# Kernel tuning notes

Hardware: AMD Instinct MI355X
Metric: run time of the kernel (lower is better)

The kernel has to match this reference:

```python
import jax, jax.numpy as jnp
import numpy as np

B, N, NPOINT, NSAMPLE = 16, 4096, 1024, 32
IN_CH = 3
MLP = [64, 64, 128]
EPS = 1e-5


def setup_inputs() -> dict:
    key = jax.random.key(0)
    ks = jax.random.split(key, 16)
    inp = {
        "xyz": jax.random.normal(ks[0], (B, N, 3), jnp.float32),
        "points": jax.random.normal(ks[1], (B, N, IN_CH), jnp.float32),
        "fps_idx": jax.random.randint(ks[2], (B, NPOINT), 0, N, jnp.int64),
    }
    last = IN_CH + 3
    for li, out_ch in enumerate(MLP):
        kw, kb, kg, kt = jax.random.split(jax.random.fold_in(key, 100 + li), 4)
        inp[f"w{li}"] = jax.random.normal(kw, (out_ch, last), jnp.float32) * (1.0 / np.sqrt(last))
        inp[f"b{li}"] = jax.random.normal(kb, (out_ch,), jnp.float32) * 0.01
        inp[f"g{li}"] = 1.0 + 0.1 * jax.random.normal(kg, (out_ch,), jnp.float32)
        inp[f"t{li}"] = 0.1 * jax.random.normal(kt, (out_ch,), jnp.float32)
        last = out_ch
    return inp


def _gather(x, idx):
    # x: [B, N, C], idx: [B, ...] -> [B, ..., C]
    return jax.vmap(lambda xb, ib: xb[ib])(x, idx)


def _conv_bn_relu(x, w, b, g, t):
    # x: [B, S, K, Cin]; 1x1 conv == channel matmul; BN in training mode (batch stats)
    y = jnp.einsum('bskc,oc->bsko', x, w) + b
    mean = y.mean(axis=(0, 1, 2))
    var = y.var(axis=(0, 1, 2))  # biased, as torch BN uses for normalization
    y = (y - mean) * jax.lax.rsqrt(var + EPS) * g + t
    return jax.nn.relu(y)


def reference(xyz, points, fps_idx, w0, b0, g0, t0, w1, b1, g1, t1, w2, b2, g2, t2):
    # sample query points
    new_xyz = jnp.take_along_axis(xyz, fps_idx[..., None], axis=1)  # [B, S, 3]
    # kNN ball query: squared distances [B, S, N]
    d = (jnp.sum(new_xyz**2, -1)[:, :, None]
         + jnp.sum(xyz**2, -1)[:, None, :]
         - 2.0 * jnp.einsum('bsd,bnd->bsn', new_xyz, xyz))
    _, idx = jax.lax.top_k(-d, NSAMPLE)  # [B, S, K]
    grouped_xyz = _gather(xyz, idx)                      # [B, S, K, 3]
    normed = grouped_xyz - new_xyz[:, :, None, :]
    grouped_pts = _gather(points, idx)                   # [B, S, K, Cin]
    x = jnp.concatenate([normed, grouped_pts], axis=-1)  # [B, S, K, 3+Cin]
    x = _conv_bn_relu(x, w0, b0, g0, t0)
    x = _conv_bn_relu(x, w1, b1, g1, t1)
    x = _conv_bn_relu(x, w2, b2, g2, t2)
    feat = jnp.max(x, axis=2)  # max over nsample -> [B, S, Cout]
    return (new_xyz, feat)
```

## Files before the change

kernel.cpp:

```cpp
#include <hip/hip_runtime.h>

#define BB 16
#define NN 4096
#define SS 1024
#define KK 32
#define MPTS (BB*SS*KK)
#define EPSF 1e-5f
#define CANDCAP 512
#define NARROW 48

#define OFF_QP    0
#define OFF_P4    (OFF_QP + BB*SS*4)
#define OFF_ST    (OFF_P4 + BB*NN*4)
#define OFF_MOM   (OFF_ST)
#define OFF_S1SUM (OFF_ST+32)
#define OFF_S1SQ  (OFF_ST+96)
#define OFF_S2SUM (OFF_ST+160)
#define OFF_S2SQ  (OFF_ST+288)
#define OFF_WF0   (OFF_ST+512)
#define OFF_XG    (OFF_ST+1280)
#define OFF_MAXB  (OFF_XG + 6*MPTS)
#define OFF_MINB  (OFF_MAXB + BB*SS*128)
#define OFF_Y1U   (OFF_MINB + BB*SS*128)

typedef __bf16 bf16x8 __attribute__((ext_vector_type(8)));
typedef float f32x4 __attribute__((ext_vector_type(4)));
typedef unsigned int uintx4 __attribute__((ext_vector_type(4)));

__device__ __forceinline__ unsigned rne_bf16(float f){
  unsigned u = __float_as_uint(f);
  return (u + 0x7FFFu + ((u>>16)&1u)) >> 16;
}

__global__ __launch_bounds__(256) void prep_kernel(
    const float* __restrict__ xyz, const int* __restrict__ fps,
    float* __restrict__ out, float* __restrict__ ws)
{
  const int g = blockIdx.x*256 + threadIdx.x;
  if (g < BB*NN){
    const float* p = xyz + (size_t)g*3;
    float x=p[0], y=p[1], z=p[2];
    float x2 = __fadd_rn(__fadd_rn(__fmul_rn(x,x),__fmul_rn(y,y)),__fmul_rn(z,z));
    *reinterpret_cast<float4*>(ws + OFF_P4 + (size_t)g*4) = make_float4(x,y,z,x2);
  } else {
    int j = g - BB*NN;
    if (j < BB*SS){
      int b = j >> 10;
      int idx = fps[j];
      const float* p = xyz + ((size_t)b*NN + idx)*3;
      float x=p[0], y=p[1], z=p[2];
      out[(size_t)j*3+0]=x; out[(size_t)j*3+1]=y; out[(size_t)j*3+2]=z;
      float q2 = __fadd_rn(__fadd_rn(__fmul_rn(x,x),__fmul_rn(y,y)),__fmul_rn(z,z));
      *reinterpret_cast<float4*>(ws + OFF_QP + (size_t)j*4) = make_float4(x,y,z,q2);
    }
  }
}

__global__ __launch_bounds__(256) void knn_group_kernel(
    const float* __restrict__ pts, float* __restrict__ ws)
{
  __shared__ unsigned wcnt[2][4];
  __shared__ unsigned long long cand[CANDCAP];
  __shared__ int sel[KK];
  __shared__ int sh_nlt;
  __shared__ unsigned sh_mcnt;

  const int bid = blockIdx.x;
  const int b = bid >> 10;
  const int tid = threadIdx.x;
  const int lane = tid & 63;
  const int wv = tid >> 6;

  const float4 q = *reinterpret_cast<const float4*>(ws + OFF_QP + (size_t)bid*4);
  const float qx=q.x, qy=q.y, qz=q.z, q2=q.w;
  const float4* pb = reinterpret_cast<const float4*>(ws + OFF_P4) + (size_t)b*NN;

  unsigned k[16];
  #pragma unroll
  for (int j=0;j<16;j++){
    int n = tid + j*256;
    float4 P = pb[n];
    float dot = __fadd_rn(__fadd_rn(__fmul_rn(qx,P.x),__fmul_rn(qy,P.y)),__fmul_rn(qz,P.z));
    float d = __fsub_rn(__fadd_rn(q2, P.w), __fmul_rn(2.0f,dot));
    unsigned u = __float_as_uint(d);
    k[j] = u ^ (unsigned)(((int)u>>31) | (int)0x80000000);
  }

  if (tid==0){ sh_nlt = 0; sh_mcnt = 0; }

  unsigned long long lo = 0, hi = 1ull<<32;
  unsigned clo = 0, chi = NN;
  int rounds = 0;
  while (chi - clo > NARROW && (hi - lo) > 1 && rounds < 28){
    const unsigned mid = (unsigned)((lo + hi) >> 1);
    unsigned cnt = 0;
    #pragma unroll
    for (int j=0;j<16;j++)
      cnt += (unsigned)__popcll(__ballot((int)(k[j] < mid)));
    if (lane==0) wcnt[rounds&1][wv] = cnt;
    __syncthreads();
    const unsigned c = wcnt[rounds&1][0]+wcnt[rounds&1][1]
                     + wcnt[rounds&1][2]+wcnt[rounds&1][3];
    if (c >= (unsigned)KK){ hi = mid; chi = c; } else { lo = mid; clo = c; }
    ++rounds;
  }

  const unsigned lo32 = (unsigned)lo;
  #pragma unroll
  for (int j=0;j<16;j++){
    int n = tid + j*256;
    if (k[j] < lo32){ int p = atomicAdd(&sh_nlt,1); sel[p] = n; }
    else if ((unsigned long long)k[j] < hi){
      unsigned p = atomicAdd(&sh_mcnt,1u);
      if (p < CANDCAP) cand[p] = ((unsigned long long)k[j]<<32) | (unsigned)n;
    }
  }
  __syncthreads();
  const int nlt = sh_nlt;
  const int kk = KK - nlt;
  const unsigned m = (sh_mcnt < CANDCAP) ? sh_mcnt : CANDCAP;
  for (unsigned i=tid; i<m; i+=256){
    const unsigned long long ci = cand[i];
    unsigned r = 0;
    for (unsigned jj=0; jj<m; ++jj) r += (cand[jj] < ci) ? 1u : 0u;
    if (r < (unsigned)kk) sel[nlt + (int)r] = (int)(ci & 0xFFFFFFFFu);
  }
  __syncthreads();

  if (tid < KK){
    int n = sel[tid];
    float4 P = pb[n];
    float v6[6];
    v6[0] = P.x-qx; v6[1] = P.y-qy; v6[2] = P.z-qz;
    const float* pt = pts + ((size_t)b*NN + n)*3;
    v6[3] = pt[0]; v6[4] = pt[1]; v6[5] = pt[2];
    size_t pidx = (size_t)bid*KK + tid;
    float* xg = ws + OFF_XG;
    #pragma unroll
    for (int c=0;c<6;c++) xg[(size_t)c*MPTS + pidx] = v6[c];
  }
}

__global__ __launch_bounds__(256) void mom2_kernel(float* __restrict__ ws)
{
  static const signed char C1[27]={0,1,2,3,4,5, 0,0,0,0,0,0, 1,1,1,1,1, 2,2,2,2, 3,3,3, 4,4, 5};
  static const signed char C2[27]={-1,-1,-1,-1,-1,-1, 0,1,2,3,4,5, 1,2,3,4,5, 2,3,4,5, 3,4,5, 4,5, 5};
  const int mq = blockIdx.x >> 3;
  const int sl = blockIdx.x & 7;
  const float4* xa = reinterpret_cast<const float4*>(ws + OFF_XG + (size_t)C1[mq]*MPTS) + (size_t)sl*(MPTS/32);
  const int c2 = C2[mq];
  float s = 0.f;
  if (c2 < 0){
    for (int i=threadIdx.x; i<MPTS/32; i+=256){
      float4 a = xa[i];
      s += (a.x+a.y)+(a.z+a.w);
    }
  } else {
    const float4* xb = reinterpret_cast<const float4*>(ws + OFF_XG + (size_t)c2*MPTS) + (size_t)sl*(MPTS/32);
    for (int i=threadIdx.x; i<MPTS/32; i+=256){
      float4 a = xa[i]; float4 bq = xb[i];
      s = fmaf(a.x,bq.x,s); s = fmaf(a.y,bq.y,s);
      s = fmaf(a.z,bq.z,s); s = fmaf(a.w,bq.w,s);
    }
  }
  #pragma unroll
  for (int off=32; off>=1; off>>=1) s += __shfl_xor(s,off,64);
  __shared__ float r[4];
  const int lane = threadIdx.x & 63, wv = threadIdx.x >> 6;
  if (lane==0) r[wv]=s;
  __syncthreads();
  if (threadIdx.x==0) atomicAdd(&ws[OFF_MOM+mq], r[0]+r[1]+r[2]+r[3]);
}

__global__ void finalize0b_kernel(const float* __restrict__ w0, const float* __restrict__ b0,
                                  const float* __restrict__ g0, const float* __restrict__ t0,
                                  float* __restrict__ ws)
{
  int o = threadIdx.x;
  const float* mom = ws + OFF_MOM;
  float w[6];
  #pragma unroll
  for (int c=0;c<6;c++) w[c] = w0[o*6+c];
  float bo = b0[o];
  float wS = 0.f;
  #pragma unroll
  for (int c=0;c<6;c++) wS += w[c]*mom[c];
  const float Mf = (float)MPTS;
  float mean = (wS + Mf*bo) / Mf;
  float qsum = 0.f;
  int mi = 6;
  #pragma unroll
  for (int c=0;c<6;c++){
    #pragma unroll
    for (int c2=c;c2<6;c2++){
      float f = (c==c2)?1.f:2.f;
      qsum += f * w[c]*w[c2]*mom[mi];
      mi++;
    }
  }
  float E2  = (qsum + 2.f*bo*wS + Mf*bo*bo) / Mf;
  float var = E2 - mean*mean;
  float sc  = g0[o] / sqrtf(var + EPSF);
  float sh  = t0[o] - mean*sc;
  float* wf = ws + OFF_WF0 + o*8;
  #pragma unroll
  for (int c=0;c<6;c++) wf[c] = sc*w[c];
  wf[6] = sc*bo + sh;
  wf[7] = 0.f;
}

__global__ __launch_bounds__(256) void l1_mfma_kernel(
    const float* __restrict__ w1g, const float* __restrict__ b1g,
    float* __restrict__ ws)
{
  __shared__ __align__(16) unsigned short sA1[4096];
  __shared__ float red[128];
  const int tid = threadIdx.x;
  const int lane = tid & 63;
  const int wv = tid >> 6;
  const int col = lane & 15;
  const int kg = lane >> 4;

  for (int idx=tid; idx<4096; idx+=256){
    int frag = idx>>9, l = (idx>>3)&63, j = idx&7;
    int mt = frag>>1, kt = frag&1;
    int o = mt*16 + (l&15);
    int c = kt*32 + ((l>>4)<<3) + j;
    sA1[idx] = (unsigned short)rne_bf16(w1g[o*64+c]);
  }
  if (tid<128) red[tid]=0.f;
  __syncthreads();

  const float* wf = ws + OFF_WF0;
  float cw0[2][8], cw1[2][8], cw2[2][8], cw3[2][8], cw4[2][8], cw5[2][8], cb[2][8];
  #pragma unroll
  for (int kt=0; kt<2; ++kt){
    #pragma unroll
    for (int j=0;j<8;j++){
      int c = kt*32 + kg*8 + j;
      float4 a4 = *reinterpret_cast<const float4*>(wf + c*8);
      float4 b4 = *reinterpret_cast<const float4*>(wf + c*8 + 4);
      cw0[kt][j]=a4.x; cw1[kt][j]=a4.y; cw2[kt][j]=a4.z; cw3[kt][j]=a4.w;
      cw4[kt][j]=b4.x; cw5[kt][j]=b4.y; cb[kt][j]=b4.z;
    }
  }
  float b1v[4][4];
  #pragma unroll
  for (int mt=0;mt<4;mt++)
    #pragma unroll
    for (int r=0;r<4;r++) b1v[mt][r] = b1g[mt*16 + kg*4 + r];

  float s1s[4][4], s1q[4][4];
  #pragma unroll
  for (int mt=0;mt<4;mt++)
    #pragma unroll
    for (int r=0;r<4;r++){ s1s[mt][r]=0.f; s1q[mt][r]=0.f; }

  const float* xg = ws + OFF_XG;
  unsigned short* y1 = (unsigned short*)(ws + OFF_Y1U);
  const int pbase = (blockIdx.x*4 + wv)*256;

  for (int it=0; it<16; ++it){
    const size_t p = (size_t)pbase + it*16 + col;
    const float x0 = xg[p];
    const float x1 = xg[MPTS+p];
    const float x2 = xg[2ul*MPTS+p];
    const float x3 = xg[3ul*MPTS+p];
    const float x4 = xg[4ul*MPTS+p];
    const float x5 = xg[5ul*MPTS+p];

    f32x4 acc0 = {0,0,0,0}, acc1 = {0,0,0,0}, acc2 = {0,0,0,0}, acc3 = {0,0,0,0};

    #pragma unroll
    for (int kt=0; kt<2; ++kt){
      float h[8];
      #pragma unroll
      for (int j=0;j<8;j++){
        float y = cb[kt][j];
        y = fmaf(cw0[kt][j],x0,y); y = fmaf(cw1[kt][j],x1,y);
        y = fmaf(cw2[kt][j],x2,y); y = fmaf(cw3[kt][j],x3,y);
        y = fmaf(cw4[kt][j],x4,y); y = fmaf(cw5[kt][j],x5,y);
        h[j] = fmaxf(y, 0.f);
      }
      uintx4 pk;
      pk[0] = rne_bf16(h[0]) | (rne_bf16(h[1])<<16);
      pk[1] = rne_bf16(h[2]) | (rne_bf16(h[3])<<16);
      pk[2] = rne_bf16(h[4]) | (rne_bf16(h[5])<<16);
      pk[3] = rne_bf16(h[6]) | (rne_bf16(h[7])<<16);
      bf16x8 bfrag = __builtin_bit_cast(bf16x8, pk);
      {
        uintx4 au = *reinterpret_cast<const uintx4*>(&sA1[((0*2+kt)*64+lane)*8]);
        acc0 = __builtin_amdgcn_mfma_f32_16x16x32_bf16(__builtin_bit_cast(bf16x8,au), bfrag, acc0, 0,0,0);
      }
      {
        uintx4 au = *reinterpret_cast<const uintx4*>(&sA1[((1*2+kt)*64+lane)*8]);
        acc1 = __builtin_amdgcn_mfma_f32_16x16x32_bf16(__builtin_bit_cast(bf16x8,au), bfrag, acc1, 0,0,0);
      }
      {
        uintx4 au = *reinterpret_cast<const uintx4*>(&sA1[((2*2+kt)*64+lane)*8]);
        acc2 = __builtin_amdgcn_mfma_f32_16x16x32_bf16(__builtin_bit_cast(bf16x8,au), bfrag, acc2, 0,0,0);
      }
      {
        uintx4 au = *reinterpret_cast<const uintx4*>(&sA1[((3*2+kt)*64+lane)*8]);
        acc3 = __builtin_amdgcn_mfma_f32_16x16x32_bf16(__builtin_bit_cast(bf16x8,au), bfrag, acc3, 0,0,0);
      }
    }
    #pragma unroll
    for (int mt=0;mt<4;mt++){
      f32x4 a = (mt==0)?acc0:(mt==1)?acc1:(mt==2)?acc2:acc3;
      float v0 = a[0] + b1v[mt][0];
      float v1 = a[1] + b1v[mt][1];
      float v2 = a[2] + b1v[mt][2];
      float v3 = a[3] + b1v[mt][3];
      s1s[mt][0]+=v0; s1q[mt][0]=fmaf(v0,v0,s1q[mt][0]);
      s1s[mt][1]+=v1; s1q[mt][1]=fmaf(v1,v1,s1q[mt][1]);
      s1s[mt][2]+=v2; s1q[mt][2]=fmaf(v2,v2,s1q[mt][2]);
      s1s[mt][3]+=v3; s1q[mt][3]=fmaf(v3,v3,s1q[mt][3]);
      uint2 st;
      st.x = rne_bf16(v0) | (rne_bf16(v1)<<16);
      st.y = rne_bf16(v2) | (rne_bf16(v3)<<16);
      *reinterpret_cast<uint2*>(y1 + p*64 + mt*16 + kg*4) = st;
    }
  }

  #pragma unroll
  for (int mt=0;mt<4;mt++){
    #pragma unroll
    for (int r=0;r<4;r++){
      float s = s1s[mt][r], qv = s1q[mt][r];
      s += __shfl_xor(s,1,64); s += __shfl_xor(s,2,64);
      s += __shfl_xor(s,4,64); s += __shfl_xor(s,8,64);
      qv += __shfl_xor(qv,1,64); qv += __shfl_xor(qv,2,64);
      qv += __shfl_xor(qv,4,64); qv += __shfl_xor(qv,8,64);
      if (col==0){
        atomicAdd(&red[mt*16 + kg*4 + r], s);
        atomicAdd(&red[64 + mt*16 + kg*4 + r], qv);
      }
    }
  }
  __syncthreads();
  if (tid < 64){
    atomicAdd(&ws[OFF_S1SUM+tid], red[tid]);
    atomicAdd(&ws[OFF_S1SQ+tid],  red[64+tid]);
  }
}

__global__ __launch_bounds__(256) void l2_mfma_kernel(
    const float* __restrict__ w2g, const float* __restrict__ b2g,
    const float* __restrict__ g1, const float* __restrict__ t1,
    float* __restrict__ ws)
{
  __shared__ __align__(16) unsigned short sB[8192];
  __shared__ float s1c[64], s1h[64];
  __shared__ float red[256];
  const int tid = threadIdx.x;
  for (int idx=tid; idx<8192; idx+=256){
    int nt = idx>>10, kt = (idx>>9)&1, l = (idx>>3)&63, j = idx&7;
    int kch = kt*32 + ((l>>4)<<3) + j;
    int o   = (nt<<4) + (l&15);
    sB[idx] = (unsigned short)rne_bf16(w2g[o*64+kch]);
  }
  if (tid<64){
    const float Mf = (float)MPTS;
    float mean = ws[OFF_S1SUM+tid]/Mf;
    float var  = ws[OFF_S1SQ+tid]/Mf - mean*mean;
    float sc = g1[tid]/sqrtf(var+EPSF);
    s1c[tid]=sc; s1h[tid]=t1[tid]-mean*sc;
  }
  red[tid]=0.f;
  __syncthreads();

  const int lane = tid & 63;
  const int w    = tid >> 6;
  const int col  = lane & 15;
  const int kg   = lane >> 4;

  float scv[2][8], shv[2][8];
  #pragma unroll
  for (int kt=0;kt<2;kt++)
    #pragma unroll
    for (int j=0;j<8;j++){
      scv[kt][j] = s1c[kt*32 + kg*8 + j];
      shv[kt][j] = s1h[kt*32 + kg*8 + j];
    }
  float b2v[8];
  #pragma unroll
  for (int nt=0;nt<8;nt++) b2v[nt] = b2g[nt*16 + col];

  const unsigned short* y1 = (const unsigned short*)(ws + OFF_Y1U);
  float* maxb = ws + OFF_MAXB;
  float* minb = ws + OFF_MINB;

  float sumacc[8], sqacc[8];
  #pragma unroll
  for (int nt=0;nt<8;nt++){ sumacc[nt]=0.f; sqacc[nt]=0.f; }

  const int gbase = (blockIdx.x*4 + w)*4;
  for (int it=0; it<4; ++it){
    const int g = gbase + it;
    const size_t p0 = (size_t)g*32;
    bf16x8 aA[2][2];
    #pragma unroll
    for (int mh=0; mh<2; ++mh){
      const unsigned short* arow = y1 + (p0 + mh*16 + col)*64 + kg*8;
      #pragma unroll
      for (int kt=0; kt<2; ++kt){
        uintx4 ua = *reinterpret_cast<const uintx4*>(arow + kt*32);
        float h0 = fmaxf(fmaf(scv[kt][0], __uint_as_float(ua[0]<<16),          shv[kt][0]), 0.f);
        float h1 = fmaxf(fmaf(scv[kt][1], __uint_as_float(ua[0]&0xFFFF0000u), shv[kt][1]), 0.f);
        float h2 = fmaxf(fmaf(scv[kt][2], __uint_as_float(ua[1]<<16),          shv[kt][2]), 0.f);
        float h3 = fmaxf(fmaf(scv[kt][3], __uint_as_float(ua[1]&0xFFFF0000u), shv[kt][3]), 0.f);
        float h4 = fmaxf(fmaf(scv[kt][4], __uint_as_float(ua[2]<<16),          shv[kt][4]), 0.f);
        float h5 = fmaxf(fmaf(scv[kt][5], __uint_as_float(ua[2]&0xFFFF0000u), shv[kt][5]), 0.f);
        float h6 = fmaxf(fmaf(scv[kt][6], __uint_as_float(ua[3]<<16),          shv[kt][6]), 0.f);
        float h7 = fmaxf(fmaf(scv[kt][7], __uint_as_float(ua[3]&0xFFFF0000u), shv[kt][7]), 0.f);
        uintx4 pk;
        pk[0] = rne_bf16(h0) | (rne_bf16(h1)<<16);
        pk[1] = rne_bf16(h2) | (rne_bf16(h3)<<16);
        pk[2] = rne_bf16(h4) | (rne_bf16(h5)<<16);
        pk[3] = rne_bf16(h6) | (rne_bf16(h7)<<16);
        aA[mh][kt] = __builtin_bit_cast(bf16x8, pk);
      }
    }
    f32x4 acc[2][8];
    #pragma unroll
    for (int mh=0;mh<2;mh++)
      #pragma unroll
      for (int nt=0;nt<8;nt++){
        f32x4 z = {b2v[nt], b2v[nt], b2v[nt], b2v[nt]};
        acc[mh][nt] = z;
      }
    #pragma unroll
    for (int nt=0;nt<8;nt++){
      #pragma unroll
      for (int kt=0;kt<2;kt++){
        uintx4 bu = *reinterpret_cast<const uintx4*>(&sB[((nt*2+kt)*64 + lane)*8]);
        bf16x8 bv = __builtin_bit_cast(bf16x8, bu);
        acc[0][nt] = __builtin_amdgcn_mfma_f32_16x16x32_bf16(aA[0][kt], bv, acc[0][nt], 0,0,0);
        acc[1][nt] = __builtin_amdgcn_mfma_f32_16x16x32_bf16(aA[1][kt], bv, acc[1][nt], 0,0,0);
      }
    }
    #pragma unroll
    for (int nt=0;nt<8;nt++){
      f32x4 a0 = acc[0][nt], a1 = acc[1][nt];
      float mx = fmaxf(fmaxf(fmaxf(a0[0],a0[1]),fmaxf(a0[2],a0[3])),
                       fmaxf(fmaxf(a1[0],a1[1]),fmaxf(a1[2],a1[3])));
      float mn = fminf(fminf(fminf(a0[0],a0[1]),fminf(a0[2],a0[3])),
                       fminf(fminf(a1[0],a1[1]),fminf(a1[2],a1[3])));
      mx = fmaxf(mx, __shfl_xor(mx,16,64)); mx = fmaxf(mx, __shfl_xor(mx,32,64));
      mn = fminf(mn, __shfl_xor(mn,16,64)); mn = fminf(mn, __shfl_xor(mn,32,64));
      float s = ((a0[0]+a0[1])+(a0[2]+a0[3])) + ((a1[0]+a1[1])+(a1[2]+a1[3]));
      sumacc[nt] += s;
      float qv = 0.f;
      qv = fmaf(a0[0],a0[0],qv); qv = fmaf(a0[1],a0[1],qv);
      qv = fmaf(a0[2],a0[2],qv); qv = fmaf(a0[3],a0[3],qv);
      qv = fmaf(a1[0],a1[0],qv); qv = fmaf(a1[1],a1[1],qv);
      qv = fmaf(a1[2],a1[2],qv); qv = fmaf(a1[3],a1[3],qv);
      sqacc[nt] += qv;
      if (lane < 16){
        maxb[(size_t)g*128 + nt*16 + lane] = mx;
        minb[(size_t)g*128 + nt*16 + lane] = mn;
      }
    }
  }
  #pragma unroll
  for (int nt=0;nt<8;nt++){
    float s = sumacc[nt]; s += __shfl_xor(s,16,64); s += __shfl_xor(s,32,64);
    float qv = sqacc[nt]; qv += __shfl_xor(qv,16,64); qv += __shfl_xor(qv,32,64);
    if (lane < 16){
      atomicAdd(&red[nt*16+lane], s);
      atomicAdd(&red[128+nt*16+lane], qv);
    }
  }
  __syncthreads();
  atomicAdd(&ws[OFF_S2SUM + tid], red[tid]);
}

__global__ __launch_bounds__(256) void final_out_kernel(
    const float* __restrict__ g2, const float* __restrict__ t2,
    const float* __restrict__ ws, float* __restrict__ out)
{
  const int g = blockIdx.x*256 + threadIdx.x;
  const int o = g & 127;
  const float Mf = (float)MPTS;
  float mean = ws[OFF_S2SUM+o] / Mf;
  float var  = ws[OFF_S2SQ+o] / Mf - mean*mean;
  float sc = g2[o] / sqrtf(var + EPSF);
  float sh = t2[o] - mean*sc;
  float v = (sc > 0.f) ? ws[OFF_MAXB+g] : ws[OFF_MINB+g];
  out[BB*SS*3 + g] = fmaxf(fmaf(sc, v, sh), 0.f);
}

extern "C" void kernel_launch(void* const* d_in, const int* in_sizes, int n_in,
                              void* d_out, int out_size, void* d_ws, size_t ws_size,
                              hipStream_t stream)
{
  const float* xyz = (const float*)d_in[0];
  const float* pts = (const float*)d_in[1];
  const int*   fps = (const int*)d_in[2];
  const float* w0  = (const float*)d_in[3];
  const float* b0  = (const float*)d_in[4];
  const float* g0  = (const float*)d_in[5];
  const float* t0  = (const float*)d_in[6];
  const float* w1  = (const float*)d_in[7];
  const float* b1  = (const float*)d_in[8];
  const float* g1  = (const float*)d_in[9];
  const float* t1  = (const float*)d_in[10];
  const float* w2  = (const float*)d_in[11];
  const float* b2  = (const float*)d_in[12];
  const float* g2  = (const float*)d_in[13];
  const float* t2  = (const float*)d_in[14];
  float* out = (float*)d_out;
  float* ws  = (float*)d_ws;

  hipMemsetAsync((void*)(ws + OFF_ST), 0, 512*sizeof(float), stream);
  prep_kernel<<<320,256,0,stream>>>(xyz, fps, out, ws);
  knn_group_kernel<<<BB*SS,256,0,stream>>>(pts, ws);
  mom2_kernel<<<27*8,256,0,stream>>>(ws);
  finalize0b_kernel<<<1,64,0,stream>>>(w0,b0,g0,t0,ws);
  l1_mfma_kernel<<<512,256,0,stream>>>(w1,b1,ws);
  l2_mfma_kernel<<<1024,256,0,stream>>>(w2,b2,g1,t1,ws);
  final_out_kernel<<<(BB*SS*128)/256,256,0,stream>>>(g2,t2,ws,out);
}
```

Measured before the change: 245.5 us.

## Use per-wave kNN threshold search and fold BN0 finalize into layer-1 kernel

The kNN bisection now runs independently in each wave. Each wave starts from its own min/max key range and uses ballot counts only, so the per-round shared-memory reduction and __syncthreads are gone. The union of the per-wave candidate sets is then rank-sorted to pick the global 32 nearest, which removes the separate less-than bucket. The trade-off is a larger candidate set and more quadratic rank-sort work per block. Separately, the single-block finalize0b kernel is removed and its BN0 fold is recomputed in shared memory by every l1 block, saving a launch and a global round-trip at the cost of redundant work per block.

```diff
diff --git a/kernel.cpp b/kernel.cpp
--- a/kernel.cpp
+++ b/kernel.cpp
@@ -7,7 +7,7 @@
 #define MPTS (BB*SS*KK)
 #define EPSF 1e-5f
 #define CANDCAP 512
-#define NARROW 48
+#define WNARROW 16
 
 #define OFF_QP    0
 #define OFF_P4    (OFF_QP + BB*SS*4)
@@ -17,7 +17,6 @@
 #define OFF_S1SQ  (OFF_ST+96)
 #define OFF_S2SUM (OFF_ST+160)
 #define OFF_S2SQ  (OFF_ST+288)
-#define OFF_WF0   (OFF_ST+512)
 #define OFF_XG    (OFF_ST+1280)
 #define OFF_MAXB  (OFF_XG + 6*MPTS)
 #define OFF_MINB  (OFF_MAXB + BB*SS*128)
@@ -59,17 +58,13 @@
 __global__ __launch_bounds__(256) void knn_group_kernel(
     const float* __restrict__ pts, float* __restrict__ ws)
 {
-  __shared__ unsigned wcnt[2][4];
   __shared__ unsigned long long cand[CANDCAP];
   __shared__ int sel[KK];
-  __shared__ int sh_nlt;
   __shared__ unsigned sh_mcnt;
 
   const int bid = blockIdx.x;
   const int b = bid >> 10;
   const int tid = threadIdx.x;
-  const int lane = tid & 63;
-  const int wv = tid >> 6;
 
   const float4 q = *reinterpret_cast<const float4*>(ws + OFF_QP + (size_t)bid*4);
   const float qx=q.x, qy=q.y, qz=q.z, q2=q.w;
@@ -86,44 +81,45 @@
     k[j] = u ^ (unsigned)(((int)u>>31) | (int)0x80000000);
   }
 
-  if (tid==0){ sh_nlt = 0; sh_mcnt = 0; }
-
-  unsigned long long lo = 0, hi = 1ull<<32;
-  unsigned clo = 0, chi = NN;
+  if (tid==0) sh_mcnt = 0;
+
+  unsigned mn = k[0], mx = k[0];
+  #pragma unroll
+  for (int j=1;j<16;j++){ mn = min(mn,k[j]); mx = max(mx,k[j]); }
+  #pragma unroll
+  for (int off=32; off>=1; off>>=1){
+    mn = min(mn, (unsigned)__shfl_xor(mn, off, 64));
+    mx = max(mx, (unsigned)__shfl_xor(mx, off, 64));
+  }
+
+  unsigned long long lo = mn, hi = (unsigned long long)mx + 1;
+  unsigned clo = 0, chi = 1024;
   int rounds = 0;
-  while (chi - clo > NARROW && (hi - lo) > 1 && rounds < 28){
+  while (chi - clo > WNARROW && (hi - lo) > 1 && rounds < 28){
     const unsigned mid = (unsigned)((lo + hi) >> 1);
     unsigned cnt = 0;
     #pragma unroll
     for (int j=0;j<16;j++)
       cnt += (unsigned)__popcll(__ballot((int)(k[j] < mid)));
-    if (lane==0) wcnt[rounds&1][wv] = cnt;
-    __syncthreads();
-    const unsigned c = wcnt[rounds&1][0]+wcnt[rounds&1][1]
-                     + wcnt[rounds&1][2]+wcnt[rounds&1][3];
-    if (c >= (unsigned)KK){ hi = mid; chi = c; } else { lo = mid; clo = c; }
+    if (cnt >= (unsigned)KK){ hi = mid; chi = cnt; } else { lo = mid; clo = cnt; }
     ++rounds;
   }
-
-  const unsigned lo32 = (unsigned)lo;
+  __syncthreads();
+
   #pragma unroll
   for (int j=0;j<16;j++){
-    int n = tid + j*256;
-    if (k[j] < lo32){ int p = atomicAdd(&sh_nlt,1); sel[p] = n; }
-    else if ((unsigned long long)k[j] < hi){
+    if ((unsigned long long)k[j] < hi){
       unsigned p = atomicAdd(&sh_mcnt,1u);
-      if (p < CANDCAP) cand[p] = ((unsigned long long)k[j]<<32) | (unsigned)n;
-    }
-  }
-  __syncthreads();
-  const int nlt = sh_nlt;
-  const int kk = KK - nlt;
+      if (p < CANDCAP) cand[p] = ((unsigned long long)k[j]<<32) | (unsigned)(tid + j*256);
+    }
+  }
+  __syncthreads();
   const unsigned m = (sh_mcnt < CANDCAP) ? sh_mcnt : CANDCAP;
   for (unsigned i=tid; i<m; i+=256){
     const unsigned long long ci = cand[i];
     unsigned r = 0;
     for (unsigned jj=0; jj<m; ++jj) r += (cand[jj] < ci) ? 1u : 0u;
-    if (r < (unsigned)kk) sel[nlt + (int)r] = (int)(ci & 0xFFFFFFFFu);
+    if (r < (unsigned)KK) sel[(int)r] = (int)(ci & 0xFFFFFFFFu);
   }
   __syncthreads();
 
@@ -172,48 +168,14 @@
   if (threadIdx.x==0) atomicAdd(&ws[OFF_MOM+mq], r[0]+r[1]+r[2]+r[3]);
 }
 
-__global__ void finalize0b_kernel(const float* __restrict__ w0, const float* __restrict__ b0,
-                                  const float* __restrict__ g0, const float* __restrict__ t0,
-                                  float* __restrict__ ws)
-{
-  int o = threadIdx.x;
-  const float* mom = ws + OFF_MOM;
-  float w[6];
-  #pragma unroll
-  for (int c=0;c<6;c++) w[c] = w0[o*6+c];
-  float bo = b0[o];
-  float wS = 0.f;
-  #pragma unroll
-  for (int c=0;c<6;c++) wS += w[c]*mom[c];
-  const float Mf = (float)MPTS;
-  float mean = (wS + Mf*bo) / Mf;
-  float qsum = 0.f;
-  int mi = 6;
-  #pragma unroll
-  for (int c=0;c<6;c++){
-    #pragma unroll
-    for (int c2=c;c2<6;c2++){
-      float f = (c==c2)?1.f:2.f;
-      qsum += f * w[c]*w[c2]*mom[mi];
-      mi++;
-    }
-  }
-  float E2  = (qsum + 2.f*bo*wS + Mf*bo*bo) / Mf;
-  float var = E2 - mean*mean;
-  float sc  = g0[o] / sqrtf(var + EPSF);
-  float sh  = t0[o] - mean*sc;
-  float* wf = ws + OFF_WF0 + o*8;
-  #pragma unroll
-  for (int c=0;c<6;c++) wf[c] = sc*w[c];
-  wf[6] = sc*bo + sh;
-  wf[7] = 0.f;
-}
-
 __global__ __launch_bounds__(256) void l1_mfma_kernel(
+    const float* __restrict__ w0g, const float* __restrict__ b0g,
+    const float* __restrict__ g0, const float* __restrict__ t0,
     const float* __restrict__ w1g, const float* __restrict__ b1g,
     float* __restrict__ ws)
 {
   __shared__ __align__(16) unsigned short sA1[4096];
+  __shared__ float swf[64*8];
   __shared__ float red[128];
   const int tid = threadIdx.x;
   const int lane = tid & 63;
@@ -228,18 +190,48 @@
     int c = kt*32 + ((l>>4)<<3) + j;
     sA1[idx] = (unsigned short)rne_bf16(w1g[o*64+c]);
   }
+  if (tid<64){
+    const float* mom = ws + OFF_MOM;
+    float w[6];
+    #pragma unroll
+    for (int c=0;c<6;c++) w[c] = w0g[tid*6+c];
+    float bo = b0g[tid];
+    float wS = 0.f;
+    #pragma unroll
+    for (int c=0;c<6;c++) wS += w[c]*mom[c];
+    const float Mf = (float)MPTS;
+    float mean = (wS + Mf*bo) / Mf;
+    float qsum = 0.f;
+    int mi = 6;
+    #pragma unroll
+    for (int c=0;c<6;c++){
+      #pragma unroll
+      for (int c2=c;c2<6;c2++){
+        float f = (c==c2)?1.f:2.f;
+        qsum += f * w[c]*w[c2]*mom[mi];
+        mi++;
+      }
+    }
+    float E2  = (qsum + 2.f*bo*wS + Mf*bo*bo) / Mf;
+    float var = E2 - mean*mean;
+    float sc  = g0[tid] / sqrtf(var + EPSF);
+    float sh  = t0[tid] - mean*sc;
+    #pragma unroll
+    for (int c=0;c<6;c++) swf[tid*8+c] = sc*w[c];
+    swf[tid*8+6] = sc*bo + sh;
+    swf[tid*8+7] = 0.f;
+  }
   if (tid<128) red[tid]=0.f;
   __syncthreads();
 
-  const float* wf = ws + OFF_WF0;
   float cw0[2][8], cw1[2][8], cw2[2][8], cw3[2][8], cw4[2][8], cw5[2][8], cb[2][8];
   #pragma unroll
   for (int kt=0; kt<2; ++kt){
     #pragma unroll
     for (int j=0;j<8;j++){
       int c = kt*32 + kg*8 + j;
-      float4 a4 = *reinterpret_cast<const float4*>(wf + c*8);
-      float4 b4 = *reinterpret_cast<const float4*>(wf + c*8 + 4);
+      float4 a4 = *reinterpret_cast<const float4*>(&swf[c*8]);
+      float4 b4 = *reinterpret_cast<const float4*>(&swf[c*8 + 4]);
       cw0[kt][j]=a4.x; cw1[kt][j]=a4.y; cw2[kt][j]=a4.z; cw3[kt][j]=a4.w;
       cw4[kt][j]=b4.x; cw5[kt][j]=b4.y; cb[kt][j]=b4.z;
     }
@@ -517,8 +509,7 @@
   prep_kernel<<<320,256,0,stream>>>(xyz, fps, out, ws);
   knn_group_kernel<<<BB*SS,256,0,stream>>>(pts, ws);
   mom2_kernel<<<27*8,256,0,stream>>>(ws);
-  finalize0b_kernel<<<1,64,0,stream>>>(w0,b0,g0,t0,ws);
-  l1_mfma_kernel<<<512,256,0,stream>>>(w1,b1,ws);
+  l1_mfma_kernel<<<512,256,0,stream>>>(w0,b0,g0,t0,w1,b1,ws);
   l2_mfma_kernel<<<1024,256,0,stream>>>(w2,b2,g1,t1,ws);
   final_out_kernel<<<(BB*SS*128)/256,256,0,stream>>>(g2,t2,ws,out);
 }
```

After: 251.7 us. 2.5% more time.
